# Kernel optimization log

Measured on AMD Instinct MI355X. Metric: run time of the kernel, lower is better.

## Reference

```python
import jax, jax.numpy as jnp
import numpy as np

EMBED_DIM = 1024
HEADS = 16
HEAD_DIM = EMBED_DIM // HEADS
DIST_LAMBDA = -0.1
LN_EPS = 1e-5


def setup_inputs() -> dict:
    key = jax.random.key(0)
    ks = jax.random.split(key, 16)
    B, N, D = 32, 4096, EMBED_DIM
    s = 1.0 / np.sqrt(D)
    inp = {
        "query": jax.random.normal(ks[0], (B, D), jnp.float32),
        "context": jax.random.normal(ks[1], (B, N, D), jnp.float32),
        "dist_matrix": jax.random.uniform(ks[2], (B, 1, N), jnp.float32),
        "context_mask": jax.random.randint(ks[3], (B, N), 0, 2, jnp.int32),
        "Wq": jax.random.normal(ks[4], (D, D), jnp.float32) * s,
        "bq": jnp.zeros((D,), jnp.float32),
        "Wk": jax.random.normal(ks[5], (D, D), jnp.float32) * s,
        "bk": jnp.zeros((D,), jnp.float32),
        "Wv": jax.random.normal(ks[6], (D, D), jnp.float32) * s,
        "bv": jnp.zeros((D,), jnp.float32),
        "Wo": jax.random.normal(ks[7], (D, D), jnp.float32) * s,
        "bo": jnp.zeros((D,), jnp.float32),
        "ln_gamma": jnp.ones((D,), jnp.float32),
        "ln_beta": jnp.zeros((D,), jnp.float32),
    }
    return inp


def reference(query, context, dist_matrix, context_mask,
              Wq, bq, Wk, bk, Wv, bv, Wo, bo, ln_gamma, ln_beta):
    B, N, D = context.shape
    H, hd = HEADS, HEAD_DIM
    # projections
    q = (query @ Wq + bq).reshape(B, H, hd)            # [B,H,hd] (single query)
    k = (context @ Wk + bk).reshape(B, N, H, hd)       # [B,N,H,hd]
    v = (context @ Wv + bv).reshape(B, N, H, hd)
    # scores: [B,H,N]
    scores = jnp.einsum("bhd,bnhd->bhn", q, k) / np.sqrt(hd)
    # additive Manhattan-distance bias, broadcast over heads
    scores = scores + dist_matrix * DIST_LAMBDA        # dist_matrix [B,1,N]
    # mask
    scores = jnp.where(context_mask[:, None, :] == 0, -1e9, scores)
    attn = jax.nn.softmax(scores, axis=-1)             # [B,H,N]
    attn_out = jnp.einsum("bhn,bnhd->bhd", attn, v).reshape(B, D)
    output = attn_out @ Wo + bo
    x = query + output
    # LayerNorm
    mu = jnp.mean(x, axis=-1, keepdims=True)
    var = jnp.mean((x - mu) ** 2, axis=-1, keepdims=True)
    return (x - mu) * jax.lax.rsqrt(var + LN_EPS) * ln_gamma + ln_beta
```

## Files before the change

### kernel.cpp

```cpp
#include <hip/hip_runtime.h>
#include <hip/hip_bf16.h>
#include <math.h>

#define DDIM 1024
#define NH 16
#define HDIM 64
#define SCALE 0.125f
#define DLAM -0.1f
#define LNEPS 1e-5f
#define NS 16
#define CHW 16
#define BROW 256
#define CBSTR 1032

typedef short bf16x8 __attribute__((ext_vector_type(8)));
typedef float f32x4 __attribute__((ext_vector_type(4)));

__device__ inline unsigned short f2bf(float x) {
    return __builtin_bit_cast(unsigned short, __float2bfloat16(x));
}
__device__ inline float bfhi2f(unsigned u) {
    return __builtin_bit_cast(float, u & 0xffff0000u);
}
__device__ inline float bflo2f(unsigned u) {
    return __builtin_bit_cast(float, u << 16);
}

__device__ inline void wg_barrier_lds() {
    asm volatile("s_waitcnt lgkmcnt(0)" ::: "memory");
    __builtin_amdgcn_s_barrier();
    __builtin_amdgcn_sched_barrier(0);
}

__global__ __launch_bounds__(512) void k_q(const float* __restrict__ query,
                                           const float* __restrict__ Wq,
                                           const float* __restrict__ bq,
                                           float* __restrict__ qout) {
    int b = blockIdx.x, c0 = blockIdx.y * 128;
    __shared__ float qs[DDIM];
    __shared__ float ps[512];
    int t = threadIdx.x;
    for (int i = t; i < DDIM; i += 512) qs[i] = query[b * DDIM + i];
    __syncthreads();
    int cl = t & 127;
    int col = c0 + cl;
    int d0 = (t >> 7) * 256;
    float acc = 0.f;
#pragma unroll 8
    for (int d = d0; d < d0 + 256; ++d)
        acc = fmaf(qs[d], Wq[(size_t)d * DDIM + col], acc);
    ps[t] = acc;
    __syncthreads();
    if (t < 128)
        qout[b * DDIM + col] = ps[t] + ps[t + 128] + ps[t + 256] + ps[t + 384] + bq[col];
}

__global__ __launch_bounds__(256) void k_qp(const float* __restrict__ qin,
                                            const float* __restrict__ Wk,
                                            unsigned short* __restrict__ qpb) {
    int dt = blockIdx.x, bg = blockIdx.y;
    __shared__ float qs[8][DDIM];
    for (int i = threadIdx.x; i < 8 * DDIM; i += 256)
        qs[i >> 10][i & 1023] =
            qin[(size_t)(bg * 8 + (i >> 10)) * DDIM + (i & 1023)];
    __syncthreads();
    int h = threadIdx.x & 15, dl = threadIdx.x >> 4;
    int d = dt * 16 + dl;
    const float* wr = Wk + (size_t)d * DDIM + h * HDIM;
    float acc[8] = {0.f, 0.f, 0.f, 0.f, 0.f, 0.f, 0.f, 0.f};
#pragma unroll
    for (int j = 0; j < HDIM; ++j) {
        float wv = wr[j];
#pragma unroll
        for (int bb = 0; bb < 8; ++bb)
            acc[bb] = fmaf(wv, qs[bb][h * HDIM + j], acc[bb]);
    }
#pragma unroll
    for (int bb = 0; bb < 8; ++bb)
        qpb[((size_t)((bg * 8 + bb) * NH + h)) * DDIM + d] = f2bf(acc[bb] * SCALE);
}

__global__ __launch_bounds__(512) void k_sb(const float* __restrict__ qin,
                                            const float* __restrict__ bk,
                                            float* __restrict__ sb) {
    int idx = threadIdx.x;
    int b = idx >> 4, h = idx & 15;
    float acc = 0.f;
#pragma unroll
    for (int j = 0; j < HDIM; ++j)
        acc = fmaf(bk[h * HDIM + j], qin[b * DDIM + h * HDIM + j], acc);
    sb[idx] = acc * SCALE;
}

__global__ __launch_bounds__(256, 2) void k_flash2(
    const float* __restrict__ ctx, const unsigned short* __restrict__ qpb,
    const float* __restrict__ sb, const float* __restrict__ dist,
    const int* __restrict__ mask, float* __restrict__ partA,
    float* __restrict__ partM, float* __restrict__ partL, int N) {
    __shared__ unsigned short cbuf[2][CHW][CBSTR];
    __shared__ float red[4][CHW][17];
    __shared__ float P_lds[CHW][20];
    __shared__ float fh_lds[NH];
    __shared__ float dls[BROW];

    int b = blockIdx.x, ns = blockIdx.y;
    int t = threadIdx.x, lane = t & 63, w = t >> 6;
    int m = lane & 15, g = lane >> 4;
    int nb0 = ns * BROW;
    const int NIT = BROW / CHW;

    {
        float dv = dist[(size_t)b * N + nb0 + t] * DLAM;
        dls[t] = mask[(size_t)b * N + nb0 + t] ? dv : -1e30f;
    }
    bf16x8 qf[8];
#pragma unroll
    for (int j = 0; j < 8; ++j)
        qf[j] = *reinterpret_cast<const bf16x8*>(
            qpb + ((size_t)(b * NH + m)) * DDIM + w * 256 + j * 32 + g * 8);
    float sbv = sb[b * NH + m];

    f32x4 acc[NH];
#pragma unroll
    for (int h = 0; h < NH; ++h) acc[h] = (f32x4){0.f, 0.f, 0.f, 0.f};
    float m_run = -1e30f, l_run = 0.f;

    const float4* cb4 = reinterpret_cast<const float4*>(ctx) +
                        ((size_t)b * N + nb0) * (DDIM / 4);
    float4 inflight[16];

#define LOADC(c)                                                  \
    {                                                             \
        const float4* src = cb4 + (size_t)(c) * CHW * (DDIM / 4); \
        _Pragma("unroll") for (int i = 0; i < 16; ++i)            \
            inflight[i] = src[i * 256 + t];                       \
    }
#define LOAD4(qq, c)                                                  \
    {                                                                 \
        const float4* src = cb4 + (size_t)(c) * CHW * (DDIM / 4);     \
        _Pragma("unroll") for (int i = (qq) * 4; i < (qq) * 4 + 4; ++i) \
            inflight[i] = src[i * 256 + t];                           \
    }
#define WRITECB(buf)                                                         \
    {                                                                        \
        _Pragma("unroll") for (int i = 0; i < 16; ++i) {                     \
            float4 v = inflight[i];                                          \
            unsigned lo = (unsigned)f2bf(v.x) | ((unsigned)f2bf(v.y) << 16); \
            unsigned hi = (unsigned)f2bf(v.z) | ((unsigned)f2bf(v.w) << 16); \
            *reinterpret_cast<uint2*>(&cbuf[buf][i][t * 4]) =                \
                make_uint2(lo, hi);                                          \
        }                                                                    \
    }
#define WRITE4(qq, buf)                                                      \
    {                                                                        \
        _Pragma("unroll") for (int i = (qq) * 4; i < (qq) * 4 + 4; ++i) {    \
            float4 v = inflight[i];                                          \
            unsigned lo = (unsigned)f2bf(v.x) | ((unsigned)f2bf(v.y) << 16); \
            unsigned hi = (unsigned)f2bf(v.z) | ((unsigned)f2bf(v.w) << 16); \
            *reinterpret_cast<uint2*>(&cbuf[buf][i][t * 4]) =                \
                make_uint2(lo, hi);                                          \
        }                                                                    \
    }

    LOADC(0);
    WRITECB(0);
    LOADC(1);

    int dq = w * 256 + lane * 4;
    for (int c = 0; c < NIT; ++c) {
        wg_barrier_lds();
        int buf = c & 1;
        if (c + 2 < NIT) {
#pragma unroll
            for (int q = 0; q < 4; ++q) {
                WRITE4(q, buf ^ 1);
                __builtin_amdgcn_sched_barrier(0);
                LOAD4(q, c + 2);
                __builtin_amdgcn_sched_barrier(0);
            }
        } else if (c + 1 < NIT) {
            WRITECB(buf ^ 1);
        }
        f32x4 cS = {0.f, 0.f, 0.f, 0.f};
#pragma unroll
        for (int j = 0; j < 8; ++j) {
            bf16x8 a = *reinterpret_cast<const bf16x8*>(
                &cbuf[buf][m][w * 256 + j * 32 + g * 8]);
            cS = __builtin_amdgcn_mfma_f32_16x16x32_bf16(a, qf[j], cS, 0, 0, 0);
        }
#pragma unroll
        for (int r = 0; r < 4; ++r) red[w][g * 4 + r][m] = cS[r];
        wg_barrier_lds();
        float S[4];
#pragma unroll
        for (int r = 0; r < 4; ++r) {
            int n = g * 4 + r;
            S[r] = red[0][n][m] + red[1][n][m] + red[2][n][m] + red[3][n][m] +
                   sbv + dls[c * CHW + n];
        }
        float cm = fmaxf(fmaxf(S[0], S[1]), fmaxf(S[2], S[3]));
        cm = fmaxf(cm, __shfl_xor(cm, 16, 64));
        cm = fmaxf(cm, __shfl_xor(cm, 32, 64));
        float mnew = fmaxf(m_run, cm);
        float f = __expf(m_run - mnew);
        float p[4];
        float ls = 0.f;
#pragma unroll
        for (int r = 0; r < 4; ++r) {
            p[r] = __expf(S[r] - mnew);
            ls += p[r];
        }
        ls += __shfl_xor(ls, 16, 64);
        ls += __shfl_xor(ls, 32, 64);
        l_run = l_run * f + ls;
        m_run = mnew;
#pragma unroll
        for (int r = 0; r < 4; ++r) P_lds[g * 4 + r][m] = p[r];
        if (w == 0 && g == 0) fh_lds[m] = f;
        wg_barrier_lds();
#pragma unroll
        for (int h = 0; h < NH; ++h) acc[h] *= fh_lds[h];
#pragma unroll 4
        for (int n = 0; n < CHW; ++n) {
            uint2 cw = *reinterpret_cast<const uint2*>(&cbuf[buf][n][dq]);
            float cv0 = bflo2f(cw.x), cv1 = bfhi2f(cw.x);
            float cv2 = bflo2f(cw.y), cv3 = bfhi2f(cw.y);
            float4 P0 = *reinterpret_cast<const float4*>(&P_lds[n][0]);
            float4 P1 = *reinterpret_cast<const float4*>(&P_lds[n][4]);
            float4 P2 = *reinterpret_cast<const float4*>(&P_lds[n][8]);
            float4 P3 = *reinterpret_cast<const float4*>(&P_lds[n][12]);
            float Pv[16] = {P0.x, P0.y, P0.z, P0.w, P1.x, P1.y, P1.z, P1.w,
                            P2.x, P2.y, P2.z, P2.w, P3.x, P3.y, P3.z, P3.w};
#pragma unroll
            for (int h = 0; h < NH; ++h) {
                acc[h][0] = fmaf(Pv[h], cv0, acc[h][0]);
                acc[h][1] = fmaf(Pv[h], cv1, acc[h][1]);
                acc[h][2] = fmaf(Pv[h], cv2, acc[h][2]);
                acc[h][3] = fmaf(Pv[h], cv3, acc[h][3]);
            }
        }
    }

#pragma unroll
    for (int h = 0; h < NH; ++h) {
        float4 o = make_float4(acc[h][0], acc[h][1], acc[h][2], acc[h][3]);
        *reinterpret_cast<float4*>(
            partA + ((size_t)((b * NS + ns) * NH + h)) * DDIM + dq) = o;
    }
    if (t < NH) {
        partM[(b * NS + ns) * NH + t] = m_run;
        partL[(b * NS + ns) * NH + t] = l_run;
    }
#undef LOADC
#undef LOAD4
#undef WRITECB
#undef WRITE4
}

__global__ __launch_bounds__(256) void k_comb(const float* __restrict__ partA,
                                              const float* __restrict__ partM,
                                              const float* __restrict__ partL,
                                              float* __restrict__ ctxa) {
    int row = blockIdx.x;
    int b = row >> 4, h = row & 15;
    float M = -1e30f;
#pragma unroll
    for (int ns = 0; ns < NS; ++ns)
        M = fmaxf(M, partM[(b * NS + ns) * NH + h]);
    float denom = 0.f;
#pragma unroll
    for (int ns = 0; ns < NS; ++ns)
        denom = fmaf(__expf(partM[(b * NS + ns) * NH + h] - M),
                     partL[(b * NS + ns) * NH + h], denom);
    float inv = 1.f / denom;
    int d4 = threadIdx.x * 4;
    float4 a = make_float4(0.f, 0.f, 0.f, 0.f);
#pragma unroll 8
    for (int ns = 0; ns < NS; ++ns) {
        float wv = __expf(partM[(b * NS + ns) * NH + h] - M);
        float4 v = *reinterpret_cast<const float4*>(
            partA + ((size_t)((b * NS + ns) * NH + h)) * DDIM + d4);
        a.x = fmaf(wv, v.x, a.x);
        a.y = fmaf(wv, v.y, a.y);
        a.z = fmaf(wv, v.z, a.z);
        a.w = fmaf(wv, v.w, a.w);
    }
    float4 o = make_float4(a.x * inv, a.y * inv, a.z * inv, a.w * inv);
    *reinterpret_cast<float4*>(ctxa + (size_t)row * DDIM + d4) = o;
}

__global__ __launch_bounds__(256) void k_vproj(const float* __restrict__ ctxa,
                                               const float* __restrict__ Wv,
                                               const float* __restrict__ bv,
                                               float* __restrict__ oattn) {
    int b = blockIdx.x, c0 = blockIdx.y * 128;
    int h0 = c0 >> 6;
    __shared__ float cs[2][DDIM];
    __shared__ float ps[256];
    for (int i = threadIdx.x; i < 2 * DDIM; i += 256)
        cs[i >> 10][i & 1023] =
            ctxa[((size_t)(b * NH + h0 + (i >> 10))) * DDIM + (i & 1023)];
    __syncthreads();
    int t = threadIdx.x;
    int cl = t & 127;
    int col = c0 + cl;
    int hl = cl >> 6;
    int d0 = (t >> 7) * 512;
    float acc = 0.f;
#pragma unroll 8
    for (int d = d0; d < d0 + 512; ++d)
        acc = fmaf(cs[hl][d], Wv[(size_t)d * DDIM + col], acc);
    ps[t] = acc;
    __syncthreads();
    if (t < 128) oattn[b * DDIM + col] = ps[t] + ps[t + 128] + bv[col];
}

__global__ __launch_bounds__(256) void k_oproj(const float* __restrict__ query,
                                               const float* __restrict__ oattn,
                                               const float* __restrict__ Wo,
                                               const float* __restrict__ bo,
                                               float* __restrict__ x) {
    int b = blockIdx.x, c0 = blockIdx.y * 128;
    __shared__ float os[DDIM];
    __shared__ float ps[256];
    for (int i = threadIdx.x; i < DDIM; i += 256) os[i] = oattn[b * DDIM + i];
    __syncthreads();
    int t = threadIdx.x;
    int col = c0 + (t & 127);
    int d0 = (t >> 7) * 512;
    float acc = 0.f;
#pragma unroll 8
    for (int d = d0; d < d0 + 512; ++d)
        acc = fmaf(os[d], Wo[(size_t)d * DDIM + col], acc);
    ps[t] = acc;
    __syncthreads();
    if (t < 128)
        x[b * DDIM + col] = query[b * DDIM + col] + ps[t] + ps[t + 128] + bo[col];
}

__global__ __launch_bounds__(256) void k_ln(const float* __restrict__ x,
                                            const float* __restrict__ gamma,
                                            const float* __restrict__ beta,
                                            float* __restrict__ out) {
    int b = blockIdx.x;
    int t = threadIdx.x;
    __shared__ float red[8];
    float xv[4];
    float lsum = 0.f;
#pragma unroll
    for (int k = 0; k < 4; ++k) {
        xv[k] = x[b * DDIM + t + k * 256];
        lsum += xv[k];
    }
#pragma unroll
    for (int off = 32; off > 0; off >>= 1) lsum += __shfl_xor(lsum, off, 64);
    if ((t & 63) == 0) red[t >> 6] = lsum;
    __syncthreads();
    float mu = (red[0] + red[1] + red[2] + red[3]) * (1.f / DDIM);
    float lsq = 0.f;
#pragma unroll
    for (int k = 0; k < 4; ++k) {
        float dx = xv[k] - mu;
        lsq += dx * dx;
    }
#pragma unroll
    for (int off = 32; off > 0; off >>= 1) lsq += __shfl_xor(lsq, off, 64);
    if ((t & 63) == 0) red[4 + (t >> 6)] = lsq;
    __syncthreads();
    float var = (red[4] + red[5] + red[6] + red[7]) * (1.f / DDIM);
    float rstd = rsqrtf(var + LNEPS);
#pragma unroll
    for (int k = 0; k < 4; ++k) {
        int c = t + k * 256;
        out[b * DDIM + c] = (xv[k] - mu) * rstd * gamma[c] + beta[c];
    }
}

extern "C" void kernel_launch(void* const* d_in, const int* in_sizes, int n_in,
                              void* d_out, int out_size, void* d_ws, size_t ws_size,
                              hipStream_t stream) {
    const float* query = (const float*)d_in[0];
    const float* ctx   = (const float*)d_in[1];
    const float* dist  = (const float*)d_in[2];
    const int*   mask  = (const int*)d_in[3];
    const float* Wq = (const float*)d_in[4];
    const float* bq = (const float*)d_in[5];
    const float* Wk = (const float*)d_in[6];
    const float* bk = (const float*)d_in[7];
    const float* Wv = (const float*)d_in[8];
    const float* bv = (const float*)d_in[9];
    const float* Wo = (const float*)d_in[10];
    const float* bo = (const float*)d_in[11];
    const float* gamma = (const float*)d_in[12];
    const float* beta  = (const float*)d_in[13];
    float* out = (float*)d_out;

    int B = in_sizes[0] / DDIM;
    int N = in_sizes[1] / (B * DDIM);

    float* ws = (float*)d_ws;
    float* q = ws;
    unsigned short* qpb = (unsigned short*)(q + (size_t)B * DDIM);
    float* sb = (float*)(qpb + (size_t)B * NH * DDIM);
    float* partA = sb + (size_t)B * NH;
    float* partM = partA + (size_t)B * NS * NH * DDIM;
    float* partL = partM + (size_t)B * NS * NH;
    float* ctxa = partL + (size_t)B * NS * NH;
    float* oattn = ctxa + (size_t)B * NH * DDIM;
    float* xbuf = oattn + (size_t)B * DDIM;

    k_q<<<dim3(B, 8), 512, 0, stream>>>(query, Wq, bq, q);
    k_qp<<<dim3(DDIM / 16, B / 8), 256, 0, stream>>>(q, Wk, qpb);
    k_sb<<<1, B * NH, 0, stream>>>(q, bk, sb);
    k_flash2<<<dim3(B, NS), 256, 0, stream>>>(ctx, qpb, sb, dist, mask,
                                              partA, partM, partL, N);
    k_comb<<<B * NH, 256, 0, stream>>>(partA, partM, partL, ctxa);
    k_vproj<<<dim3(B, 8), 256, 0, stream>>>(ctxa, Wv, bv, oattn);
    k_oproj<<<dim3(B, 8), 256, 0, stream>>>(query, oattn, Wo, bo, xbuf);
    k_ln<<<B, 256, 0, stream>>>(xbuf, gamma, beta, out);
}
```

Baseline: 241.4 us.

## Compute P·V accumulation with bf16 MFMA instead of scalar FMAs via LDS

Replaces the scalar FMA loop that computed softmax-weight times context products with 16x16x32 bf16 MFMA instructions. P values stay in registers as the A operand and are zero-padded to K=32, so the P_lds/fh_lds round trip and one workgroup barrier per chunk go away. The rescale factors are now broadcast with lane shuffles. In exchange, half of each MFMA's K dimension is wasted, B operands are gathered with scalar 16-bit LDS reads, P is rounded to bf16, and partial outputs are written with strided scalar stores.

```diff
diff --git a/kernel.cpp b/kernel.cpp
--- a/kernel.cpp
+++ b/kernel.cpp
@@ -19,12 +19,6 @@
 __device__ inline unsigned short f2bf(float x) {
     return __builtin_bit_cast(unsigned short, __float2bfloat16(x));
 }
-__device__ inline float bfhi2f(unsigned u) {
-    return __builtin_bit_cast(float, u & 0xffff0000u);
-}
-__device__ inline float bflo2f(unsigned u) {
-    return __builtin_bit_cast(float, u << 16);
-}
 
 __device__ inline void wg_barrier_lds() {
     asm volatile("s_waitcnt lgkmcnt(0)" ::: "memory");
@@ -99,8 +93,6 @@
     float* __restrict__ partM, float* __restrict__ partL, int N) {
     __shared__ unsigned short cbuf[2][CHW][CBSTR];
     __shared__ float red[4][CHW][17];
-    __shared__ float P_lds[CHW][20];
-    __shared__ float fh_lds[NH];
     __shared__ float dls[BROW];
 
     int b = blockIdx.x, ns = blockIdx.y;
@@ -120,9 +112,9 @@
             qpb + ((size_t)(b * NH + m)) * DDIM + w * 256 + j * 32 + g * 8);
     float sbv = sb[b * NH + m];
 
-    f32x4 acc[NH];
-#pragma unroll
-    for (int h = 0; h < NH; ++h) acc[h] = (f32x4){0.f, 0.f, 0.f, 0.f};
+    f32x4 acc[16];
+#pragma unroll
+    for (int td = 0; td < 16; ++td) acc[td] = (f32x4){0.f, 0.f, 0.f, 0.f};
     float m_run = -1e30f, l_run = 0.f;
 
     const float4* cb4 = reinterpret_cast<const float4*>(ctx) +
@@ -166,7 +158,7 @@
     WRITECB(0);
     LOADC(1);
 
-    int dq = w * 256 + lane * 4;
+    int dcol = lane & 15;
     for (int c = 0; c < NIT; ++c) {
         wg_barrier_lds();
         int buf = c & 1;
@@ -214,38 +206,41 @@
         ls += __shfl_xor(ls, 32, 64);
         l_run = l_run * f + ls;
         m_run = mnew;
-#pragma unroll
-        for (int r = 0; r < 4; ++r) P_lds[g * 4 + r][m] = p[r];
-        if (w == 0 && g == 0) fh_lds[m] = f;
-        wg_barrier_lds();
-#pragma unroll
-        for (int h = 0; h < NH; ++h) acc[h] *= fh_lds[h];
-#pragma unroll 4
-        for (int n = 0; n < CHW; ++n) {
-            uint2 cw = *reinterpret_cast<const uint2*>(&cbuf[buf][n][dq]);
-            float cv0 = bflo2f(cw.x), cv1 = bfhi2f(cw.x);
-            float cv2 = bflo2f(cw.y), cv3 = bfhi2f(cw.y);
-            float4 P0 = *reinterpret_cast<const float4*>(&P_lds[n][0]);
-            float4 P1 = *reinterpret_cast<const float4*>(&P_lds[n][4]);
-            float4 P2 = *reinterpret_cast<const float4*>(&P_lds[n][8]);
-            float4 P3 = *reinterpret_cast<const float4*>(&P_lds[n][12]);
-            float Pv[16] = {P0.x, P0.y, P0.z, P0.w, P1.x, P1.y, P1.z, P1.w,
-                            P2.x, P2.y, P2.z, P2.w, P3.x, P3.y, P3.z, P3.w};
-#pragma unroll
-            for (int h = 0; h < NH; ++h) {
-                acc[h][0] = fmaf(Pv[h], cv0, acc[h][0]);
-                acc[h][1] = fmaf(Pv[h], cv1, acc[h][1]);
-                acc[h][2] = fmaf(Pv[h], cv2, acc[h][2]);
-                acc[h][3] = fmaf(Pv[h], cv3, acc[h][3]);
-            }
-        }
-    }
-
-#pragma unroll
-    for (int h = 0; h < NH; ++h) {
-        float4 o = make_float4(acc[h][0], acc[h][1], acc[h][2], acc[h][3]);
-        *reinterpret_cast<float4*>(
-            partA + ((size_t)((b * NS + ns) * NH + h)) * DDIM + dq) = o;
+        bf16x8 pa = (bf16x8){0, 0, 0, 0, 0, 0, 0, 0};
+        pa[0] = (short)f2bf(p[0]);
+        pa[1] = (short)f2bf(p[1]);
+        pa[2] = (short)f2bf(p[2]);
+        pa[3] = (short)f2bf(p[3]);
+        float fr[4];
+#pragma unroll
+        for (int r = 0; r < 4; ++r) fr[r] = __shfl(f, (lane >> 4) * 4 + r, 64);
+#pragma unroll
+        for (int td = 0; td < 16; ++td) {
+            acc[td][0] *= fr[0];
+            acc[td][1] *= fr[1];
+            acc[td][2] *= fr[2];
+            acc[td][3] *= fr[3];
+        }
+#pragma unroll
+        for (int td = 0; td < 16; ++td) {
+            int dc = w * 256 + td * 16 + dcol;
+            bf16x8 bb = (bf16x8){0, 0, 0, 0, 0, 0, 0, 0};
+            bb[0] = (short)cbuf[buf][g * 4 + 0][dc];
+            bb[1] = (short)cbuf[buf][g * 4 + 1][dc];
+            bb[2] = (short)cbuf[buf][g * 4 + 2][dc];
+            bb[3] = (short)cbuf[buf][g * 4 + 3][dc];
+            acc[td] = __builtin_amdgcn_mfma_f32_16x16x32_bf16(pa, bb, acc[td], 0, 0, 0);
+        }
+    }
+
+#pragma unroll
+    for (int td = 0; td < 16; ++td) {
+#pragma unroll
+        for (int r = 0; r < 4; ++r) {
+            int h = g * 4 + r;
+            partA[((size_t)((b * NS + ns) * NH + h)) * DDIM + w * 256 + td * 16 +
+                  dcol] = acc[td][r];
+        }
     }
     if (t < NH) {
         partM[(b * NS + ns) * NH + t] = m_run;
```

New measurement: 234.0 us. -3.1%, faster.
